# Kernel optimization log

Measured on AMD Instinct MI355X. Metric: run time of the kernel, lower is better.

## Reference

```python
import jax, jax.numpy as jnp
import numpy as np

B, C, H, W = 8, 256, 56, 56
K = 3  # kernel size


def _unfold3x3(x):
    """torch nn.Unfold(kernel=3, stride=1, pad=1) -> [B, HW, C*9].

    torch orders the unfolded channel dim as (c, ki, kj) with c slowest.
    """
    b, c, h, w = x.shape
    xp = jnp.pad(x, ((0, 0), (0, 0), (1, 1), (1, 1)))
    # stack 9 shifted views -> [B, C, 9, H, W]
    patches = jnp.stack(
        [xp[:, :, i:i + h, j:j + w] for i in range(K) for j in range(K)],
        axis=2,
    )
    return patches.reshape(b, c * K * K, h * w).transpose(0, 2, 1)


def setup_inputs() -> dict:
    key = jax.random.key(0)
    ks = jax.random.split(key, 8)
    d = C * K * K  # 2304
    s1 = 1.0 / np.sqrt(d)
    s2 = 1.0 / np.sqrt(C)
    return {
        "x": jax.random.normal(ks[0], (B, C, H, W), jnp.float32),
        "W1": jax.random.uniform(ks[1], (d, C), jnp.float32, -s1, s1),
        "b1": jax.random.uniform(ks[2], (C,), jnp.float32, -s1, s1),
        "W2": jax.random.uniform(ks[3], (C, d), jnp.float32, -s2, s2),
        "b2": jax.random.uniform(ks[4], (d,), jnp.float32, -s2, s2),
        "W3": jax.random.uniform(ks[5], (d, C), jnp.float32, -s1, s1),
        "b3": jax.random.uniform(ks[6], (C,), jnp.float32, -s1, s1),
    }


def reference(x, W1, b1, W2, b2, W3, b3):
    t = _unfold3x3(x)                                   # [B, HW, C*9]
    h1 = jax.nn.relu(jnp.einsum('bld,dc->blc', t, W1) + b1)   # [B, HW, C]
    s = jax.nn.sigmoid(jnp.einsum('blc,cd->bld', h1, W2) + b2)  # [B, HW, C*9]
    out = jnp.einsum('bld,dc->blc', t * s, W3) + b3     # [B, HW, C]
    return out
```

## Files before the change

kernel.cpp:

```cpp
#include <hip/hip_runtime.h>

typedef unsigned short u16;
typedef unsigned int u32;
typedef __attribute__((ext_vector_type(8))) short bfrag_t;
typedef __attribute__((ext_vector_type(4))) float accfrag_t;
typedef __attribute__((ext_vector_type(4))) u32 u32x4;

__device__ __forceinline__ u16 f2b(float f) {
    u32 u = __float_as_uint(f);
    u32 r = (u + 0x7FFFu + ((u >> 16) & 1u)) >> 16;
    return (u16)r;
}
__device__ __forceinline__ u32 pkbf16(float lo, float hi) {
    u32 r;
    asm("v_cvt_pk_bf16_f32 %0, %1, %2" : "=v"(r) : "v"(lo), "v"(hi));
    return r;
}
__device__ __forceinline__ float blo(u32 v) { return __uint_as_float(v << 16); }
__device__ __forceinline__ float bhi(u32 v) { return __uint_as_float(v & 0xffff0000u); }

__device__ __forceinline__ void load16(const u16* g, u16* l) {
    __builtin_amdgcn_global_load_lds(
        (__attribute__((address_space(1))) void*)(u16*)g,
        (__attribute__((address_space(3))) void*)l,
        16, 0, 0);
}

__global__ __launch_bounds__(256) void k_prep(
    const float* __restrict__ x, const float* __restrict__ W1,
    const float* __restrict__ W2, const float* __restrict__ W3,
    const float* __restrict__ b2, u16* __restrict__ xtp,
    u16* __restrict__ W1f, u16* __restrict__ W2f,
    u16* __restrict__ W3f, float* __restrict__ b2p) {
    __shared__ __align__(16) char smem[29184];
    const int bid = blockIdx.x;
    const int tid = threadIdx.x;
    if (bid < 928) {
        const int b = bid / 116;
        const int r = bid - b * 116;
        const int hp = r >> 1;
        const int ch = r & 1;
        u16* rowbase = xtp + (size_t)(b * 58 + hp) * 58 * 256;
        if (hp == 0 || hp == 57) {
            if (ch == 0) {
                u32* p = (u32*)rowbase;
                for (int i = tid; i < 58 * 128; i += 256) p[i] = 0;
            }
            return;
        }
        float* lds = (float*)smem;
        const int h = hp - 1;
        const int c0 = ch * 128;
        const float* xb = x + (size_t)(b * 256 + c0) * 3136 + h * 56;
#pragma unroll
        for (int it = 0; it < 7; ++it) {
            const int idx = it * 256 + tid;
            const int cl = idx / 14;
            const int f4 = idx - cl * 14;
            const float4 v = *(const float4*)(xb + (size_t)cl * 3136 + f4 * 4);
            float* d = lds + cl * 57 + f4 * 4;
            d[0] = v.x; d[1] = v.y; d[2] = v.z; d[3] = v.w;
        }
        __syncthreads();
        u32* orow = (u32*)rowbase;
        const int cp = tid & 63;
        const int wg = tid >> 6;
        const float* l0p = lds + (2 * cp) * 57;
        const float* l1p = lds + (2 * cp + 1) * 57;
#pragma unroll
        for (int it = 0; it < 15; ++it) {
            const int wp = it * 4 + wg;
            if (wp < 58) {
                u32 val = 0;
                if (wp >= 1 && wp <= 56) val = pkbf16(l0p[wp - 1], l1p[wp - 1]);
                orow[wp * 128 + ch * 64 + cp] = val;
            }
        }
    } else if (bid < 1072) {
        int b = bid - 928;
        const float* in = b < 72 ? W1 : W3;
        u16* out = b < 72 ? W1f : W3f;
        if (b >= 72) b -= 72;
        const int rrp = b >> 3;
        const int cg = b & 7;
        u16* lds1 = (u16*)smem;
#pragma unroll
        for (int cc = 0; cc < 32; ++cc) {
            int d = (cg * 32 + cc) * 9 + rrp;
            lds1[cc * 256 + tid] = f2b(in[d * 256 + tid]);
        }
        __syncthreads();
        const int kc72 = rrp * 8 + cg;
#pragma unroll
        for (int s = 0; s < 32; ++s) {
            const int w = s >> 2;
            const int o = (s & 3) * 256 + tid;
            const int e = o & 7;
            const int ln = (o >> 3) & 63;
            const int j = o >> 9;
            const int n = w * 32 + j * 16 + (ln & 15);
            const int q = (ln >> 4) * 8 + e;
            out[(w * 72 + kc72) * 1024 + o] = lds1[q * 256 + n];
        }
    } else if (bid < 1144) {
        const int b = bid - 1072;
        const int rr = b >> 3;
        const int w = b & 7;
        u16* lds2 = (u16*)smem;
#pragma unroll
        for (int s = 0; s < 32; ++s) {
            int li = s * 256 + tid;
            int k = li >> 5, dloc = li & 31;
            lds2[k * 32 + dloc] = f2b(W2[k * 2304 + (w * 32 + dloc) * 9 + rr]);
        }
        __syncthreads();
        u16* ob = W2f + (rr * 8 + w) * 8192;
#pragma unroll
        for (int s = 0; s < 32; ++s) {
            const int o = s * 256 + tid;
            const int e = o & 7;
            const int ln = (o >> 3) & 63;
            const int j = (o >> 9) & 1;
            const int kc = o >> 10;
            const int k = kc * 32 + (ln >> 4) * 8 + e;
            const int dloc = j * 16 + (ln & 15);
            ob[o] = lds2[k * 32 + dloc];
        }
    } else {
        int idx = (bid - 1144) * 256 + tid;
        if (idx < 2304) b2p[idx] = b2[(idx & 255) * 9 + (idx >> 8)];
    }
}

__global__ __launch_bounds__(512, 4) void k_fused(
    const u16* __restrict__ xtp, const u16* __restrict__ W1f,
    const u16* __restrict__ W2f, const u16* __restrict__ W3f,
    const float* __restrict__ b1, const float* __restrict__ b2p,
    const float* __restrict__ b3, float* __restrict__ out) {
    __shared__ __align__(16) u16 As[16384];
    __shared__ __align__(16) u16 Us[16384];

    const int tid = threadIdx.x;
    const int wave = tid >> 6;
    const int lane = tid & 63;
    const int fr = lane & 15;
    const int fq = lane >> 4;
    const int l0 = blockIdx.x * 64;

    const int swz = (lane & 3) ^ ((lane >> 3) & 3);
    int roffs[4], ldst[4];
#pragma unroll
    for (int q = 0; q < 4; ++q) {
        const int row = q * 16 + (lane >> 2);
        const int l = l0 + row;
        const int b = l / 3136;
        const int rem = l - b * 3136;
        const int h = rem / 56;
        const int w = rem - h * 56;
        roffs[q] = ((b * 58 + h + 1) * 58 + (w + 1)) * 256 + wave * 32 + swz * 8;
        ldst[q] = wave * 2048 + (q * 64 + lane) * 8;
    }
    const int aoff = fr * 32 + ((fq ^ ((fr >> 1) & 3)) * 8);
    auto shiftOf = [](int rr) { return ((rr / 3 - 1) * 58 + (rr % 3) - 1) * 256; };
    auto stage = [&](u16* buf, int shift) {
#pragma unroll
        for (int q = 0; q < 4; ++q)
            load16(xtp + roffs[q] + shift, buf + ldst[q]);
    };
    auto ewidx = [&](int i, int j, int r) {
        const int row = i * 16 + fq * 4 + r;
        const int sl = (j * 2 + (fr >> 3)) ^ ((fq * 2 + (r >> 1)) & 3);
        return row * 32 + sl * 8 + (fr & 7);
    };

    accfrag_t acc[4][2], accO[4][2];
#pragma unroll
    for (int i = 0; i < 4; ++i)
#pragma unroll
        for (int j = 0; j < 2; ++j) {
            acc[i][j] = (accfrag_t)0.f;
            accO[i][j] = (accfrag_t)0.f;
        }

    const u16* w1p = W1f + wave * 73728 + lane * 8;
    stage(As, shiftOf(0));
    for (int rr = 0; rr < 9; ++rr) {
        u16* cur = (rr & 1) ? Us : As;
        u16* nxt = (rr & 1) ? As : Us;
        __syncthreads();
        if (rr < 8) stage(nxt, shiftOf(rr + 1));
        __builtin_amdgcn_s_setprio(1);
#pragma unroll
        for (int kc = 0; kc < 8; ++kc) {
            bfrag_t bf[2], af[4];
#pragma unroll
            for (int j = 0; j < 2; ++j)
                bf[j] = *(const bfrag_t*)(w1p + ((rr * 8 + kc) * 2 + j) * 512);
#pragma unroll
            for (int i = 0; i < 4; ++i)
                af[i] = *(const bfrag_t*)(cur + kc * 2048 + i * 512 + aoff);
#pragma unroll
            for (int i = 0; i < 4; ++i)
#pragma unroll
                for (int j = 0; j < 2; ++j)
                    acc[i][j] = __builtin_amdgcn_mfma_f32_16x16x32_bf16(
                        af[i], bf[j], acc[i][j], 0, 0, 0);
        }
        __builtin_amdgcn_s_setprio(0);
    }
    __syncthreads();
#pragma unroll
    for (int i = 0; i < 4; ++i) {
#pragma unroll
        for (int j = 0; j < 2; ++j) {
            const float bv = b1[wave * 32 + j * 16 + fr];
#pragma unroll
            for (int r = 0; r < 4; ++r) {
                float v = acc[i][j][r] + bv;
                v = v > 0.f ? v : 0.f;
                const float vh = __shfl_down(v, 1);
                if (!(lane & 1))
                    *(u32*)&As[wave * 2048 + ewidx(i, j, r)] = pkbf16(v, vh);
            }
        }
    }
    __syncthreads();

    const u16* w3p = W3f + wave * 73728 + lane * 8;
    const u16* w2base = W2f + (wave)*8192 + lane * 8;
    for (int rr = 0; rr < 9; ++rr) {
        __builtin_amdgcn_s_setprio(1);
        if (rr > 0) {
#pragma unroll
            for (int kc = 0; kc < 8; ++kc) {
                bfrag_t bf[2], af[4];
#pragma unroll
                for (int j = 0; j < 2; ++j)
                    bf[j] = *(const bfrag_t*)(w3p + (((rr - 1) * 8 + kc) * 2 + j) * 512);
#pragma unroll
                for (int i = 0; i < 4; ++i)
                    af[i] = *(const bfrag_t*)(Us + kc * 2048 + i * 512 + aoff);
#pragma unroll
                for (int i = 0; i < 4; ++i)
#pragma unroll
                    for (int j = 0; j < 2; ++j)
                        accO[i][j] = __builtin_amdgcn_mfma_f32_16x16x32_bf16(
                            af[i], bf[j], accO[i][j], 0, 0, 0);
            }
        }
        const int shift = shiftOf(rr);
        u32x4 tvreg[4];
#pragma unroll
        for (int q = 0; q < 4; ++q)
            tvreg[q] = *(const u32x4*)(xtp + roffs[q] + shift);
#pragma unroll
        for (int i = 0; i < 4; ++i)
#pragma unroll
            for (int j = 0; j < 2; ++j) acc[i][j] = (accfrag_t)0.f;
        const u16* w2p = w2base + rr * 8 * 8192;
#pragma unroll
        for (int kc = 0; kc < 8; ++kc) {
            bfrag_t bf[2], af[4];
#pragma unroll
            for (int j = 0; j < 2; ++j)
                bf[j] = *(const bfrag_t*)(w2p + (kc * 2 + j) * 512);
#pragma unroll
            for (int i = 0; i < 4; ++i)
                af[i] = *(const bfrag_t*)(As + kc * 2048 + i * 512 + aoff);
#pragma unroll
            for (int i = 0; i < 4; ++i)
#pragma unroll
                for (int j = 0; j < 2; ++j)
                    acc[i][j] = __builtin_amdgcn_mfma_f32_16x16x32_bf16(
                        af[i], bf[j], acc[i][j], 0, 0, 0);
        }
        __builtin_amdgcn_s_setprio(0);
        __syncthreads();
#pragma unroll
        for (int i = 0; i < 4; ++i) {
#pragma unroll
            for (int j = 0; j < 2; ++j) {
                const float bv = b2p[rr * 256 + wave * 32 + j * 16 + fr];
#pragma unroll
                for (int r = 0; r < 4; ++r) {
                    const float z = acc[i][j][r] + bv;
                    const float s = __builtin_amdgcn_rcpf(1.f + __expf(-z));
                    const float sh = __shfl_down(s, 1);
                    if (!(lane & 1))
                        *(u32*)&Us[wave * 2048 + ewidx(i, j, r)] = pkbf16(s, sh);
                }
            }
        }
#pragma unroll
        for (int q = 0; q < 4; ++q) {
            u32x4 sv = *(const u32x4*)(Us + ldst[q]);
            u32x4 rv;
#pragma unroll
            for (int e = 0; e < 4; ++e)
                rv[e] = pkbf16(blo(sv[e]) * blo(tvreg[q][e]),
                               bhi(sv[e]) * bhi(tvreg[q][e]));
            *(u32x4*)(Us + ldst[q]) = rv;
        }
        __syncthreads();
    }
    __builtin_amdgcn_s_setprio(1);
#pragma unroll
    for (int kc = 0; kc < 8; ++kc) {
        bfrag_t bf[2], af[4];
#pragma unroll
        for (int j = 0; j < 2; ++j)
            bf[j] = *(const bfrag_t*)(w3p + ((8 * 8 + kc) * 2 + j) * 512);
#pragma unroll
        for (int i = 0; i < 4; ++i)
            af[i] = *(const bfrag_t*)(Us + kc * 2048 + i * 512 + aoff);
#pragma unroll
        for (int i = 0; i < 4; ++i)
#pragma unroll
            for (int j = 0; j < 2; ++j)
                accO[i][j] = __builtin_amdgcn_mfma_f32_16x16x32_bf16(
                    af[i], bf[j], accO[i][j], 0, 0, 0);
    }
    __builtin_amdgcn_s_setprio(0);

#pragma unroll
    for (int i = 0; i < 4; ++i) {
#pragma unroll
        for (int j = 0; j < 2; ++j) {
            const int col = wave * 32 + j * 16 + fr;
            const float bv = b3[col];
#pragma unroll
            for (int r = 0; r < 4; ++r) {
                const float v = accO[i][j][r] + bv;
                const float vh = __shfl_down(v, 1);
                if (!(lane & 1)) {
                    float2 st = make_float2(v, vh);
                    *(float2*)(out + (size_t)(l0 + i * 16 + fq * 4 + r) * 256 + col) = st;
                }
            }
        }
    }
}

extern "C" void kernel_launch(void* const* d_in, const int* in_sizes, int n_in,
                              void* d_out, int out_size, void* d_ws, size_t ws_size,
                              hipStream_t stream) {
    const float* x  = (const float*)d_in[0];
    const float* W1 = (const float*)d_in[1];
    const float* b1 = (const float*)d_in[2];
    const float* W2 = (const float*)d_in[3];
    const float* b2 = (const float*)d_in[4];
    const float* W3 = (const float*)d_in[5];
    const float* b3 = (const float*)d_in[6];
    float* out = (float*)d_out;

    char* ws = (char*)d_ws;
    u16* xtp = (u16*)ws;  ws += (size_t)8 * 58 * 58 * 256 * 2;
    u16* W1f = (u16*)ws;  ws += (size_t)589824 * 2;
    u16* W2f = (u16*)ws;  ws += (size_t)589824 * 2;
    u16* W3f = (u16*)ws;  ws += (size_t)589824 * 2;
    float* b2p = (float*)ws;

    k_prep<<<1153, 256, 0, stream>>>(x, W1, W2, W3, b2, xtp, W1f, W2f, W3f, b2p);
    k_fused<<<392, 512, 0, stream>>>(xtp, W1f, W2f, W3f, b1, b2p, b3, out);
}
```

Baseline: 206.9 us.

## Double-buffer W2 accumulators to overlap next GEMM with sigmoid and W3 stage

Restructures the per-slice loop so the W2 GEMM for the next 3x3 offset runs into a second accumulator set while the current slice's sigmoid/gating and W3 GEMM proceed, with the x tile for the next offset prefetched after the W3 step. This aims to hide MFMA latency behind elementwise work and reduce sync stalls. It costs extra accumulator registers, which may hurt occupancy. The prep kernel is also launched twice, adding redundant work.

```diff
diff --git a/kernel.cpp b/kernel.cpp
--- a/kernel.cpp
+++ b/kernel.cpp
@@ -173,7 +173,7 @@
         return row * 32 + sl * 8 + (fr & 7);
     };
 
-    accfrag_t acc[4][2], accO[4][2];
+    accfrag_t acc[4][2], accB[4][2], accO[4][2];
 #pragma unroll
     for (int i = 0; i < 4; ++i)
 #pragma unroll
@@ -227,37 +227,16 @@
     __syncthreads();
 
     const u16* w3p = W3f + wave * 73728 + lane * 8;
-    const u16* w2base = W2f + (wave)*8192 + lane * 8;
-    for (int rr = 0; rr < 9; ++rr) {
+    const u16* w2base = W2f + wave * 8192 + lane * 8;
+    u32x4 tvreg[4];
+
+    auto do2a = [&](int rrn, accfrag_t(&a)[4][2]) {
+#pragma unroll
+        for (int i = 0; i < 4; ++i)
+#pragma unroll
+            for (int j = 0; j < 2; ++j) a[i][j] = (accfrag_t)0.f;
+        const u16* w2p = w2base + rrn * 8 * 8192;
         __builtin_amdgcn_s_setprio(1);
-        if (rr > 0) {
-#pragma unroll
-            for (int kc = 0; kc < 8; ++kc) {
-                bfrag_t bf[2], af[4];
-#pragma unroll
-                for (int j = 0; j < 2; ++j)
-                    bf[j] = *(const bfrag_t*)(w3p + (((rr - 1) * 8 + kc) * 2 + j) * 512);
-#pragma unroll
-                for (int i = 0; i < 4; ++i)
-                    af[i] = *(const bfrag_t*)(Us + kc * 2048 + i * 512 + aoff);
-#pragma unroll
-                for (int i = 0; i < 4; ++i)
-#pragma unroll
-                    for (int j = 0; j < 2; ++j)
-                        accO[i][j] = __builtin_amdgcn_mfma_f32_16x16x32_bf16(
-                            af[i], bf[j], accO[i][j], 0, 0, 0);
-            }
-        }
-        const int shift = shiftOf(rr);
-        u32x4 tvreg[4];
-#pragma unroll
-        for (int q = 0; q < 4; ++q)
-            tvreg[q] = *(const u32x4*)(xtp + roffs[q] + shift);
-#pragma unroll
-        for (int i = 0; i < 4; ++i)
-#pragma unroll
-            for (int j = 0; j < 2; ++j) acc[i][j] = (accfrag_t)0.f;
-        const u16* w2p = w2base + rr * 8 * 8192;
 #pragma unroll
         for (int kc = 0; kc < 8; ++kc) {
             bfrag_t bf[2], af[4];
@@ -271,11 +250,12 @@
             for (int i = 0; i < 4; ++i)
 #pragma unroll
                 for (int j = 0; j < 2; ++j)
-                    acc[i][j] = __builtin_amdgcn_mfma_f32_16x16x32_bf16(
-                        af[i], bf[j], acc[i][j], 0, 0, 0);
+                    a[i][j] = __builtin_amdgcn_mfma_f32_16x16x32_bf16(
+                        af[i], bf[j], a[i][j], 0, 0, 0);
         }
         __builtin_amdgcn_s_setprio(0);
-        __syncthreads();
+    };
+    auto dosig = [&](int rr, accfrag_t(&a)[4][2]) {
 #pragma unroll
         for (int i = 0; i < 4; ++i) {
 #pragma unroll
@@ -283,7 +263,7 @@
                 const float bv = b2p[rr * 256 + wave * 32 + j * 16 + fr];
 #pragma unroll
                 for (int r = 0; r < 4; ++r) {
-                    const float z = acc[i][j][r] + bv;
+                    const float z = a[i][j][r] + bv;
                     const float s = __builtin_amdgcn_rcpf(1.f + __expf(-z));
                     const float sh = __shfl_down(s, 1);
                     if (!(lane & 1))
@@ -291,6 +271,8 @@
                 }
             }
         }
+    };
+    auto doU = [&]() {
 #pragma unroll
         for (int q = 0; q < 4; ++q) {
             u32x4 sv = *(const u32x4*)(Us + ldst[q]);
@@ -301,26 +283,52 @@
                                bhi(sv[e]) * bhi(tvreg[q][e]));
             *(u32x4*)(Us + ldst[q]) = rv;
         }
-        __syncthreads();
-    }
-    __builtin_amdgcn_s_setprio(1);
-#pragma unroll
-    for (int kc = 0; kc < 8; ++kc) {
-        bfrag_t bf[2], af[4];
-#pragma unroll
-        for (int j = 0; j < 2; ++j)
-            bf[j] = *(const bfrag_t*)(w3p + ((8 * 8 + kc) * 2 + j) * 512);
-#pragma unroll
-        for (int i = 0; i < 4; ++i)
-            af[i] = *(const bfrag_t*)(Us + kc * 2048 + i * 512 + aoff);
-#pragma unroll
-        for (int i = 0; i < 4; ++i)
+    };
+    auto do2b = [&](int rr) {
+        __builtin_amdgcn_s_setprio(1);
+#pragma unroll
+        for (int kc = 0; kc < 8; ++kc) {
+            bfrag_t bf[2], af[4];
 #pragma unroll
             for (int j = 0; j < 2; ++j)
-                accO[i][j] = __builtin_amdgcn_mfma_f32_16x16x32_bf16(
-                    af[i], bf[j], accO[i][j], 0, 0, 0);
-    }
-    __builtin_amdgcn_s_setprio(0);
+                bf[j] = *(const bfrag_t*)(w3p + ((rr * 8 + kc) * 2 + j) * 512);
+#pragma unroll
+            for (int i = 0; i < 4; ++i)
+                af[i] = *(const bfrag_t*)(Us + kc * 2048 + i * 512 + aoff);
+#pragma unroll
+            for (int i = 0; i < 4; ++i)
+#pragma unroll
+                for (int j = 0; j < 2; ++j)
+                    accO[i][j] = __builtin_amdgcn_mfma_f32_16x16x32_bf16(
+                        af[i], bf[j], accO[i][j], 0, 0, 0);
+        }
+        __builtin_amdgcn_s_setprio(0);
+    };
+
+    do2a(0, acc);
+#pragma unroll
+    for (int q = 0; q < 4; ++q)
+        tvreg[q] = *(const u32x4*)(xtp + roffs[q] + shiftOf(0));
+
+    for (int rr = 0; rr < 9; ++rr) {
+        __syncthreads();
+        if ((rr & 1) == 0) {
+            dosig(rr, acc);
+            if (rr < 8) do2a(rr + 1, accB);
+        } else {
+            dosig(rr, accB);
+            if (rr < 8) do2a(rr + 1, acc);
+        }
+        doU();
+        __syncthreads();
+        do2b(rr);
+        if (rr < 8) {
+            const int shift = shiftOf(rr + 1);
+#pragma unroll
+            for (int q = 0; q < 4; ++q)
+                tvreg[q] = *(const u32x4*)(xtp + roffs[q] + shift);
+        }
+    }
 
 #pragma unroll
     for (int i = 0; i < 4; ++i) {
@@ -361,5 +369,6 @@
     float* b2p = (float*)ws;
 
     k_prep<<<1153, 256, 0, stream>>>(x, W1, W2, W3, b2, xtp, W1f, W2f, W3f, b2p);
+    k_prep<<<1153, 256, 0, stream>>>(x, W1, W2, W3, b2, xtp, W1f, W2f, W3f, b2p);
     k_fused<<<392, 512, 0, stream>>>(xtp, W1f, W2f, W3f, b1, b2p, b3, out);
 }
```

Result: slower. 330.4 us (+59.7%).
